# Kernel optimization log

Hardware: AMD Instinct MI355X
Metric: run time of the kernel (lower is better)

## Reference

```python
import jax, jax.numpy as jnp
import numpy as np

B, NUM_OBJ, R, D, C = 1024, 128, 32, 512, 7  # scans, obj slots, rel samples, feat dim, rel classes
N = NUM_OBJ + R  # 160 graph nodes per scan


def setup_inputs() -> dict:
    key = jax.random.key(0)
    ks = jax.random.split(key, 8)
    obj_feats = jax.random.normal(ks[0], (B, NUM_OBJ, D), jnp.float32)
    pairs = jax.random.randint(ks[1], (B, R, 2), 0, NUM_OBJ, dtype=jnp.int32)
    init = lambda k, shape, fan_in: jax.random.normal(k, shape, jnp.float32) / np.float32(np.sqrt(fan_in))
    return {
        "obj_feats": obj_feats,
        "pairs": pairs,
        "fuse_w": init(ks[2], (2 * D, D), 2 * D), "fuse_b": jnp.zeros((D,), jnp.float32),
        "gcn_w": init(ks[3], (D, D), D), "gcn_b": jnp.zeros((D,), jnp.float32),
        "fc1_w": init(ks[4], (D, 256), D), "fc1_b": jnp.zeros((256,), jnp.float32),
        "fc2_w": init(ks[5], (256, 128), 256), "fc2_b": jnp.zeros((128,), jnp.float32),
        "fc3_w": init(ks[6], (128, C), 128), "fc3_b": jnp.zeros((C,), jnp.float32),
    }


def reference(obj_feats, pairs, fuse_w, fuse_b, gcn_w, gcn_b,
              fc1_w, fc1_b, fc2_w, fc2_b, fc3_w, fc3_b):
    # --- init_rel_node (pos_fuse=False): fuse sub/obj features per sampled pair ---
    sub = jnp.take_along_axis(obj_feats, pairs[:, :, 0:1], axis=1)  # [B,R,D]
    obj = jnp.take_along_axis(obj_feats, pairs[:, :, 1:2], axis=1)  # [B,R,D]
    init_rel = jnp.concatenate([sub, obj], axis=-1) @ fuse_w + fuse_b  # [B,R,D]

    # --- X: object node feats in rows [0,NUM_OBJ), rel node feats in rows [NUM_OBJ,N) ---
    X = jnp.concatenate([obj_feats, init_rel], axis=1)  # [B,N,D]

    # --- A: get_graph_gcn_with_rel -- scatter 4 directed edges per pair ---
    b_idx = jnp.arange(B)[:, None]                      # [B,1]
    ridx = NUM_OBJ + jnp.arange(R)[None, :]             # [1,R] rel node index j+num_obj
    p0, p1 = pairs[:, :, 0], pairs[:, :, 1]             # [B,R]
    A = jnp.zeros((B, N, N), jnp.float32)
    A = A.at[b_idx, p0, ridx].set(1.0)
    A = A.at[b_idx, ridx, p1].set(1.0)
    A = A.at[b_idx, p1, ridx].set(1.0)
    A = A.at[b_idx, ridx, p0].set(1.0)

    # --- simpleGCN: relu((A @ X) W + b) ---
    H = jax.nn.relu(jnp.einsum('bnm,bmd->bnd', A, X) @ gcn_w + gcn_b)  # [B,N,D]

    # --- residual: GCN rel-node output + init rel feats ---
    rel_feat = H[:, NUM_OBJ:, :] + init_rel  # [B,R,D]

    # --- proxi_detector (dropout = identity, eval behavior) ---
    h = jax.nn.relu(rel_feat @ fc1_w + fc1_b)
    h = jax.nn.relu(h @ fc2_w + fc2_b)
    logits = h @ fc3_w + fc3_b  # [B,R,C]
    return jax.nn.softmax(logits, axis=-1)
```

## Files before the change

### kernel.cpp

```cpp
#include <hip/hip_runtime.h>
#include <hip/hip_bf16.h>

#define B_    1024
#define NOBJ  128
#define RREL  32
#define DIM   512
#define MTOT  32768

typedef __bf16 bf16x8 __attribute__((ext_vector_type(8)));
typedef float  f32x4  __attribute__((ext_vector_type(4)));
typedef unsigned short us;

__device__ __forceinline__ us f2bf(float f) {
    unsigned int u = __float_as_uint(f);
    u += 0x7FFFu + ((u >> 16) & 1u);
    return (us)(u >> 16);
}
__device__ __forceinline__ float bf2f(us h) {
    return __uint_as_float(((unsigned int)h) << 16);
}

__device__ __forceinline__ void load16_to_lds(const us* g, us* l) {
    __builtin_amdgcn_global_load_lds((const __attribute__((address_space(1))) void*)g,
                                     (__attribute__((address_space(3))) void*)l,
                                     16, 0, 0);
}

__global__ __launch_bounds__(256) void gather_kernel(
        const float* __restrict__ obj, const int* __restrict__ pairs,
        us* __restrict__ As, us* __restrict__ Msum) {
    int t = threadIdx.x;
    int g = t >> 7;
    int c = t & 127;
    int base = blockIdx.x * 8;
#pragma unroll
    for (int rr = 0; rr < 4; ++rr) {
        int m  = base + rr * 2 + g;
        int b  = m >> 5;
        int p0 = pairs[(m << 1) + 0];
        int p1 = pairs[(m << 1) + 1];
        const float4* srow = (const float4*)(obj + (size_t)(b * NOBJ + p0) * DIM);
        const float4* orow = (const float4*)(obj + (size_t)(b * NOBJ + p1) * DIM);
        float4 s4 = srow[c];
        float4 o4 = orow[c];
        size_t arow = (size_t)m * 1024;
        ushort4 sb = make_ushort4(f2bf(s4.x), f2bf(s4.y), f2bf(s4.z), f2bf(s4.w));
        ushort4 ob = make_ushort4(f2bf(o4.x), f2bf(o4.y), f2bf(o4.z), f2bf(o4.w));
        *(ushort4*)(As + arow + c * 4)       = sb;
        *(ushort4*)(As + arow + 512 + c * 4) = ob;
        float4 mz = s4;
        if (p0 != p1) { mz.x += o4.x; mz.y += o4.y; mz.z += o4.z; mz.w += o4.w; }
        *(ushort4*)(Msum + (size_t)m * 512 + c * 4) =
            make_ushort4(f2bf(mz.x), f2bf(mz.y), f2bf(mz.z), f2bf(mz.w));
    }
}

__global__ __launch_bounds__(256) void prep_weights(
        const float* __restrict__ fw, const float* __restrict__ gw,
        const float* __restrict__ w1, const float* __restrict__ w2,
        us* __restrict__ WfT, us* __restrict__ WgT,
        us* __restrict__ W1T, us* __restrict__ W2T) {
    __shared__ float t32[32][33];
    int id = blockIdx.x;
    const float* in; us* out; int K, N, local;
    if (id < 512)      { in = fw; out = WfT; K = 1024; N = 512; local = id; }
    else if (id < 768) { in = gw; out = WgT; K = 512;  N = 512; local = id - 512; }
    else if (id < 896) { in = w1; out = W1T; K = 512;  N = 256; local = id - 768; }
    else               { in = w2; out = W2T; K = 256;  N = 128; local = id - 896; }
    int tilesN = N >> 5;
    int bk = (local / tilesN) * 32;
    int bn = (local % tilesN) * 32;
    int t  = threadIdx.x;
    int tx = t & 31, ty = t >> 5;
#pragma unroll
    for (int i = 0; i < 4; ++i)
        t32[ty + i * 8][tx] = in[(size_t)(bk + ty + i * 8) * N + bn + tx];
    __syncthreads();
#pragma unroll
    for (int i = 0; i < 4; ++i)
        out[(size_t)(bn + ty + i * 8) * K + bk + tx] = f2bf(t32[tx][ty + i * 8]);
}

__global__ __launch_bounds__(512, 2) void gemm_fused12(
        const us* __restrict__ As,
        const us* __restrict__ Msum,
        const us* __restrict__ WfT,
        const us* __restrict__ WgT,
        const float* __restrict__ fuse_b, const float* __restrict__ gcn_b,
        us* __restrict__ rf) {
    __shared__ __align__(16) us ldsA[2][4096];
    __shared__ __align__(16) us ldsB[2][16384];

    int tid  = threadIdx.x;
    int wid  = tid >> 6;
    int lane = tid & 63;
    int wm   = wid >> 2;
    int wn   = wid & 3;
    int m0   = blockIdx.x * 128;

    f32x4 acc[4][8];
#pragma unroll
    for (int i = 0; i < 4; ++i)
#pragma unroll
        for (int j = 0; j < 8; ++j)
#pragma unroll
            for (int k = 0; k < 4; ++k) acc[i][j][k] = 0.0f;

    int r = tid >> 2, c = tid & 3;
    const us* aG = Msum + (size_t)(m0 + r) * 512  + c * 8;
    const us* aF = As   + (size_t)(m0 + r) * 1024 + c * 8;

    int l15  = lane & 15;
    int koff = (lane >> 4) * 8;
    int aoff = (wm * 64  + l15) * 32 + koff;
    int boff = (wn * 128 + l15) * 32 + koff;

    float bg_[8], bf_[8];
#pragma unroll
    for (int j = 0; j < 8; ++j) {
        int col = wn * 128 + j * 16 + l15;
        bg_[j] = gcn_b[col];
        bf_[j] = fuse_b[col];
    }

    auto stageG = [&](int ks, int buf) {
        load16_to_lds(aG + ks * 32, &ldsA[buf][tid * 8]);
#pragma unroll
        for (int q = 0; q < 4; ++q)
            load16_to_lds(WgT + (size_t)(q * 128 + r) * 512 + ks * 32 + c * 8,
                          &ldsB[buf][q * 4096 + tid * 8]);
    };
    auto stageF = [&](int ks, int buf) {
        load16_to_lds(aF + ks * 32, &ldsA[buf][tid * 8]);
#pragma unroll
        for (int q = 0; q < 4; ++q)
            load16_to_lds(WfT + (size_t)(q * 128 + r) * 1024 + ks * 32 + c * 8,
                          &ldsB[buf][q * 4096 + tid * 8]);
    };
    auto compute = [&](int buf) {
        bf16x8 a[4], b[8];
#pragma unroll
        for (int i = 0; i < 4; ++i)
            a[i] = *(const bf16x8*)(&ldsA[buf][aoff + i * 512]);
#pragma unroll
        for (int j = 0; j < 8; ++j)
            b[j] = *(const bf16x8*)(&ldsB[buf][boff + j * 512]);
#pragma unroll
        for (int i = 0; i < 4; ++i)
#pragma unroll
            for (int j = 0; j < 8; ++j)
                acc[i][j] = __builtin_amdgcn_mfma_f32_16x16x32_bf16(a[i], b[j], acc[i][j], 0, 0, 0);
    };

    int cur = 0;
    stageG(0, 0);
    __syncthreads();

    for (int s = 0; s < 16; ++s) {
        if (s < 15) stageG(s + 1, cur ^ 1);
        else        stageF(0, cur ^ 1);
        compute(cur);
        if (s == 15) {
#pragma unroll
            for (int i = 0; i < 4; ++i)
#pragma unroll
                for (int j = 0; j < 8; ++j)
#pragma unroll
                    for (int k = 0; k < 4; ++k)
                        acc[i][j][k] = fmaxf(acc[i][j][k] + bg_[j], 0.0f);
        }
        __syncthreads();
        cur ^= 1;
    }
    for (int s = 0; s < 32; ++s) {
        if (s < 31) stageF(s + 1, cur ^ 1);
        compute(cur);
        __syncthreads();
        cur ^= 1;
    }

    int crow = wm * 64 + (lane >> 4) * 4;
#pragma unroll
    for (int i = 0; i < 4; ++i)
#pragma unroll
        for (int j = 0; j < 8; ++j) {
            int col = wn * 128 + j * 16 + l15;
#pragma unroll
            for (int jj = 0; jj < 4; ++jj) {
                int row = m0 + crow + i * 16 + jj;
                rf[(size_t)row * 512 + col] = f2bf(acc[i][j][jj] + bf_[j]);
            }
        }
}

#define H1S 264
#define H2S 136
__global__ __launch_bounds__(256, 2) void tail_kernel(
        const us* __restrict__ rf,
        const us* __restrict__ W1T,
        const us* __restrict__ W2T,
        const float* __restrict__ b1, const float* __restrict__ b2,
        const float* __restrict__ w3, const float* __restrict__ b3,
        float* __restrict__ out) {
    __shared__ __align__(16) unsigned char pool[57888];
    us*    sA   = (us*)(pool);
    us*    sB   = (us*)(pool + 4096);
    us*    sH2  = (us*)(pool);
    us*    sH1  = (us*)(pool + 20480);
    float* sRed = (float*)(pool + 20480);
    float* sW3  = (float*)(pool + 54272);
    float* sB3  = (float*)(pool + 57856);

    int tid  = threadIdx.x;
    int wid  = tid >> 6;
    int lane = tid & 63;
    int m0   = blockIdx.x * 64;

    for (int i = tid; i < 128 * 7; i += 256) sW3[i] = w3[i];
    if (tid < 7) sB3[tid] = b3[tid];

    int r = tid >> 2, c = tid & 3;
    int koff = (lane >> 4) * 8;
    int l15  = lane & 15;

    f32x4 acc1[4][4];
#pragma unroll
    for (int i = 0; i < 4; ++i)
#pragma unroll
        for (int j = 0; j < 4; ++j)
#pragma unroll
            for (int k = 0; k < 4; ++k) acc1[i][j][k] = 0.0f;

    {
        const us* ag = rf + (size_t)(m0 + r) * 512 + c * 8;
        us* la = sA + wid * 512;
        for (int k0 = 0; k0 < 512; k0 += 32) {
            __syncthreads();
            load16_to_lds(ag + k0, la);
#pragma unroll
            for (int q = 0; q < 4; ++q)
                load16_to_lds(W1T + (size_t)(q * 64 + r) * 512 + k0 + c * 8,
                              sB + q * 2048 + wid * 512);
            __syncthreads();
            bf16x8 a[4], b[4];
#pragma unroll
            for (int i = 0; i < 4; ++i)
                a[i] = *(const bf16x8*)(sA + (l15 + i * 16) * 32 + koff);
#pragma unroll
            for (int j = 0; j < 4; ++j)
                b[j] = *(const bf16x8*)(sB + (wid * 64 + j * 16 + l15) * 32 + koff);
#pragma unroll
            for (int i = 0; i < 4; ++i)
#pragma unroll
                for (int j = 0; j < 4; ++j)
                    acc1[i][j] = __builtin_amdgcn_mfma_f32_16x16x32_bf16(a[i], b[j], acc1[i][j], 0, 0, 0);
        }
    }
#pragma unroll
    for (int i = 0; i < 4; ++i)
#pragma unroll
        for (int j = 0; j < 4; ++j) {
            int col = wid * 64 + j * 16 + l15;
            float bb = b1[col];
#pragma unroll
            for (int jj = 0; jj < 4; ++jj) {
                int row = i * 16 + (lane >> 4) * 4 + jj;
                sH1[row * H1S + col] = f2bf(fmaxf(acc1[i][j][jj] + bb, 0.0f));
            }
        }

    int nw = wid & 1, kw = wid >> 1;
    f32x4 acc2[4][4];
#pragma unroll
    for (int i = 0; i < 4; ++i)
#pragma unroll
        for (int j = 0; j < 4; ++j)
#pragma unroll
            for (int k = 0; k < 4; ++k) acc2[i][j][k] = 0.0f;

    for (int t = 0; t < 4; ++t) {
        __syncthreads();
#pragma unroll
        for (int s = 0; s < 2; ++s)
#pragma unroll
            for (int q = 0; q < 2; ++q)
                load16_to_lds(W2T + (size_t)(q * 64 + r) * 256 + s * 128 + t * 32 + c * 8,
                              sB + s * 4096 + q * 2048 + wid * 512);
        __syncthreads();
        bf16x8 a[4], b[4];
#pragma unroll
        for (int i = 0; i < 4; ++i)
            a[i] = *(const bf16x8*)(sH1 + (l15 + i * 16) * H1S + kw * 128 + t * 32 + koff);
#pragma unroll
        for (int j = 0; j < 4; ++j)
            b[j] = *(const bf16x8*)(sB + kw * 4096 + (nw * 64 + j * 16 + l15) * 32 + koff);
#pragma unroll
        for (int i = 0; i < 4; ++i)
#pragma unroll
            for (int j = 0; j < 4; ++j)
                acc2[i][j] = __builtin_amdgcn_mfma_f32_16x16x32_bf16(a[i], b[j], acc2[i][j], 0, 0, 0);
    }
    __syncthreads();
    if (kw == 1) {
#pragma unroll
        for (int i = 0; i < 4; ++i)
#pragma unroll
            for (int j = 0; j < 4; ++j) {
                int col = nw * 64 + j * 16 + l15;
#pragma unroll
                for (int jj = 0; jj < 4; ++jj) {
                    int row = i * 16 + (lane >> 4) * 4 + jj;
                    sRed[row * 132 + col] = acc2[i][j][jj];
                }
            }
    }
    __syncthreads();
    if (kw == 0) {
#pragma unroll
        for (int i = 0; i < 4; ++i)
#pragma unroll
            for (int j = 0; j < 4; ++j) {
                int col = nw * 64 + j * 16 + l15;
                float bb = b2[col];
#pragma unroll
                for (int jj = 0; jj < 4; ++jj) {
                    int row = i * 16 + (lane >> 4) * 4 + jj;
                    float v = acc2[i][j][jj] + sRed[row * 132 + col] + bb;
                    sH2[row * H2S + col] = f2bf(fmaxf(v, 0.0f));
                }
            }
    }
    __syncthreads();

    int row = tid >> 2;
    int p   = tid & 3;
    float accv[7];
#pragma unroll
    for (int cc = 0; cc < 7; ++cc) accv[cc] = 0.0f;
    const us* hrow = sH2 + row * H2S + p * 32;
    for (int kk = 0; kk < 8; ++kk) {
        ushort4 u = *(const ushort4*)(hrow + kk * 4);
        float f0 = bf2f(u.x), f1 = bf2f(u.y), f2 = bf2f(u.z), f3 = bf2f(u.w);
        int k = p * 32 + kk * 4;
#pragma unroll
        for (int cc = 0; cc < 7; ++cc) {
            accv[cc] = fmaf(f0, sW3[(k + 0) * 7 + cc], accv[cc]);
            accv[cc] = fmaf(f1, sW3[(k + 1) * 7 + cc], accv[cc]);
            accv[cc] = fmaf(f2, sW3[(k + 2) * 7 + cc], accv[cc]);
            accv[cc] = fmaf(f3, sW3[(k + 3) * 7 + cc], accv[cc]);
        }
    }
#pragma unroll
    for (int cc = 0; cc < 7; ++cc) {
        accv[cc] += __shfl_xor(accv[cc], 1);
        accv[cc] += __shfl_xor(accv[cc], 2);
    }
    if (p == 0) {
        float mx = accv[0] + sB3[0];
        float lg[7];
#pragma unroll
        for (int cc = 0; cc < 7; ++cc) { lg[cc] = accv[cc] + sB3[cc]; mx = fmaxf(mx, lg[cc]); }
        float sum = 0.f;
#pragma unroll
        for (int cc = 0; cc < 7; ++cc) { lg[cc] = __expf(lg[cc] - mx); sum += lg[cc]; }
        float inv = 1.0f / sum;
#pragma unroll
        for (int cc = 0; cc < 7; ++cc) out[(size_t)(m0 + row) * 7 + cc] = lg[cc] * inv;
    }
}

extern "C" void kernel_launch(void* const* d_in, const int* in_sizes, int n_in,
                              void* d_out, int out_size, void* d_ws, size_t ws_size,
                              hipStream_t stream) {
    (void)in_sizes; (void)n_in; (void)out_size; (void)ws_size;
    const float* obj    = (const float*)d_in[0];
    const int*   pairs  = (const int*)  d_in[1];
    const float* fuse_w = (const float*)d_in[2];
    const float* fuse_b = (const float*)d_in[3];
    const float* gcn_w  = (const float*)d_in[4];
    const float* gcn_b  = (const float*)d_in[5];
    const float* fc1_w  = (const float*)d_in[6];
    const float* fc1_b  = (const float*)d_in[7];
    const float* fc2_w  = (const float*)d_in[8];
    const float* fc2_b  = (const float*)d_in[9];
    const float* fc3_w  = (const float*)d_in[10];
    const float* fc3_b  = (const float*)d_in[11];
    float* out = (float*)d_out;

    char* ws = (char*)d_ws;
    us* As   = (us*)(ws);
    us* Msum = (us*)(ws + (64u  << 20));
    us* rf   = (us*)(ws + (96u  << 20));
    us* WfT  = (us*)(ws + (128u << 20));
    us* WgT  = (us*)(ws + (129u << 20));
    us* W1T  = (us*)(ws + (130u << 20));
    us* W2T  = (us*)(ws + (131u << 20));

    gather_kernel<<<MTOT / 8, 256, 0, stream>>>(obj, pairs, As, Msum);
    prep_weights<<<928, 256, 0, stream>>>(fuse_w, gcn_w, fc1_w, fc2_w,
                                          WfT, WgT, W1T, W2T);

    gemm_fused12<<<MTOT / 128, 512, 0, stream>>>(
        As, Msum, WfT, WgT, fuse_b, gcn_b, rf);

    tail_kernel<<<MTOT / 64, 256, 0, stream>>>(
        rf, W1T, W2T, fc1_b, fc2_b, fc3_w, fc3_b, out);
}
```

Before: 444.5 us.

## Fuse pair gather and bf16 conversion into the fused GEMM A-tile loader

Removes the separate gather kernel that wrote bf16 copies of sub/obj rows and their sum to workspace. The GEMM now reads fp32 object rows through the pair indices, converts them to bf16 in registers, and writes them into LDS, with register prefetch one stage ahead. This saves a kernel launch and the round trip of the gathered matrices through global memory. In exchange the A loads become fp32 register loads plus conversion work inside the GEMM loop instead of async global-to-LDS copies, which may expose latency.

Result: faster. 425.8 us (-4.2%).

```diff
diff --git a/kernel.cpp b/kernel.cpp
--- a/kernel.cpp
+++ b/kernel.cpp
@@ -10,6 +10,7 @@
 typedef __bf16 bf16x8 __attribute__((ext_vector_type(8)));
 typedef float  f32x4  __attribute__((ext_vector_type(4)));
 typedef unsigned short us;
+typedef unsigned short us8v __attribute__((ext_vector_type(8)));
 
 __device__ __forceinline__ us f2bf(float f) {
     unsigned int u = __float_as_uint(f);
@@ -24,35 +25,6 @@
     __builtin_amdgcn_global_load_lds((const __attribute__((address_space(1))) void*)g,
                                      (__attribute__((address_space(3))) void*)l,
                                      16, 0, 0);
-}
-
-__global__ __launch_bounds__(256) void gather_kernel(
-        const float* __restrict__ obj, const int* __restrict__ pairs,
-        us* __restrict__ As, us* __restrict__ Msum) {
-    int t = threadIdx.x;
-    int g = t >> 7;
-    int c = t & 127;
-    int base = blockIdx.x * 8;
-#pragma unroll
-    for (int rr = 0; rr < 4; ++rr) {
-        int m  = base + rr * 2 + g;
-        int b  = m >> 5;
-        int p0 = pairs[(m << 1) + 0];
-        int p1 = pairs[(m << 1) + 1];
-        const float4* srow = (const float4*)(obj + (size_t)(b * NOBJ + p0) * DIM);
-        const float4* orow = (const float4*)(obj + (size_t)(b * NOBJ + p1) * DIM);
-        float4 s4 = srow[c];
-        float4 o4 = orow[c];
-        size_t arow = (size_t)m * 1024;
-        ushort4 sb = make_ushort4(f2bf(s4.x), f2bf(s4.y), f2bf(s4.z), f2bf(s4.w));
-        ushort4 ob = make_ushort4(f2bf(o4.x), f2bf(o4.y), f2bf(o4.z), f2bf(o4.w));
-        *(ushort4*)(As + arow + c * 4)       = sb;
-        *(ushort4*)(As + arow + 512 + c * 4) = ob;
-        float4 mz = s4;
-        if (p0 != p1) { mz.x += o4.x; mz.y += o4.y; mz.z += o4.z; mz.w += o4.w; }
-        *(ushort4*)(Msum + (size_t)m * 512 + c * 4) =
-            make_ushort4(f2bf(mz.x), f2bf(mz.y), f2bf(mz.z), f2bf(mz.w));
-    }
 }
 
 __global__ __launch_bounds__(256) void prep_weights(
@@ -82,8 +54,8 @@
 }
 
 __global__ __launch_bounds__(512, 2) void gemm_fused12(
-        const us* __restrict__ As,
-        const us* __restrict__ Msum,
+        const float* __restrict__ obj,
+        const int*   __restrict__ pairs,
         const us* __restrict__ WfT,
         const us* __restrict__ WgT,
         const float* __restrict__ fuse_b, const float* __restrict__ gcn_b,
@@ -107,8 +79,13 @@
             for (int k = 0; k < 4; ++k) acc[i][j][k] = 0.0f;
 
     int r = tid >> 2, c = tid & 3;
-    const us* aG = Msum + (size_t)(m0 + r) * 512  + c * 8;
-    const us* aF = As   + (size_t)(m0 + r) * 1024 + c * 8;
+    int m  = m0 + r;
+    int p0 = pairs[2 * m + 0];
+    int p1 = pairs[2 * m + 1];
+    int bi = m >> 5;
+    const float* sP = obj + (size_t)(bi * NOBJ + p0) * DIM + c * 8;
+    const float* oP = obj + (size_t)(bi * NOBJ + p1) * DIM + c * 8;
+    float osc = (p0 != p1) ? 1.0f : 0.0f;
 
     int l15  = lane & 15;
     int koff = (lane >> 4) * 8;
@@ -123,20 +100,9 @@
         bf_[j] = fuse_b[col];
     }
 
-    auto stageG = [&](int ks, int buf) {
-        load16_to_lds(aG + ks * 32, &ldsA[buf][tid * 8]);
-#pragma unroll
-        for (int q = 0; q < 4; ++q)
-            load16_to_lds(WgT + (size_t)(q * 128 + r) * 512 + ks * 32 + c * 8,
-                          &ldsB[buf][q * 4096 + tid * 8]);
-    };
-    auto stageF = [&](int ks, int buf) {
-        load16_to_lds(aF + ks * 32, &ldsA[buf][tid * 8]);
-#pragma unroll
-        for (int q = 0; q < 4; ++q)
-            load16_to_lds(WfT + (size_t)(q * 128 + r) * 1024 + ks * 32 + c * 8,
-                          &ldsB[buf][q * 4096 + tid * 8]);
-    };
+    us* aDst0 = &ldsA[0][r * 32 + c * 8];
+    us* aDst1 = &ldsA[1][r * 32 + c * 8];
+
     auto compute = [&](int buf) {
         bf16x8 a[4], b[8];
 #pragma unroll
@@ -152,15 +118,56 @@
                 acc[i][j] = __builtin_amdgcn_mfma_f32_16x16x32_bf16(a[i], b[j], acc[i][j], 0, 0, 0);
     };
 
+    {
+        float4 sa = *(const float4*)(sP);
+        float4 sb = *(const float4*)(sP + 4);
+        float4 oa = *(const float4*)(oP);
+        float4 ob = *(const float4*)(oP + 4);
+        us8v u;
+        u[0] = f2bf(fmaf(osc, oa.x, sa.x)); u[1] = f2bf(fmaf(osc, oa.y, sa.y));
+        u[2] = f2bf(fmaf(osc, oa.z, sa.z)); u[3] = f2bf(fmaf(osc, oa.w, sa.w));
+        u[4] = f2bf(fmaf(osc, ob.x, sb.x)); u[5] = f2bf(fmaf(osc, ob.y, sb.y));
+        u[6] = f2bf(fmaf(osc, ob.z, sb.z)); u[7] = f2bf(fmaf(osc, ob.w, sb.w));
+        *(us8v*)aDst0 = u;
+#pragma unroll
+        for (int q = 0; q < 4; ++q)
+            load16_to_lds(WgT + (size_t)(q * 128 + r) * 512 + c * 8,
+                          &ldsB[0][q * 4096 + tid * 8]);
+    }
+    __syncthreads();
+
     int cur = 0;
-    stageG(0, 0);
-    __syncthreads();
-
-    for (int s = 0; s < 16; ++s) {
-        if (s < 15) stageG(s + 1, cur ^ 1);
-        else        stageF(0, cur ^ 1);
+    for (int t = 0; t < 48; ++t) {
+        float4 ra, rb, rc, rd;
+        int  nt = t + 1;
+        bool hv = nt < 48;
+        bool gm = nt < 16;
+        if (hv) {
+            if (gm) {
+                int k0 = nt * 32;
+                ra = *(const float4*)(sP + k0);
+                rb = *(const float4*)(sP + k0 + 4);
+                rc = *(const float4*)(oP + k0);
+                rd = *(const float4*)(oP + k0 + 4);
+#pragma unroll
+                for (int q = 0; q < 4; ++q)
+                    load16_to_lds(WgT + (size_t)(q * 128 + r) * 512 + k0 + c * 8,
+                                  &ldsB[cur ^ 1][q * 4096 + tid * 8]);
+            } else {
+                int kf = (nt - 16) * 32;
+                const float* p = (kf < 512) ? (sP + kf) : (oP + (kf - 512));
+                ra = *(const float4*)(p);
+                rb = *(const float4*)(p + 4);
+#pragma unroll
+                for (int q = 0; q < 4; ++q)
+                    load16_to_lds(WfT + (size_t)(q * 128 + r) * 1024 + kf + c * 8,
+                                  &ldsB[cur ^ 1][q * 4096 + tid * 8]);
+            }
+        }
+
         compute(cur);
-        if (s == 15) {
+
+        if (t == 15) {
 #pragma unroll
             for (int i = 0; i < 4; ++i)
 #pragma unroll
@@ -169,12 +176,20 @@
                     for (int k = 0; k < 4; ++k)
                         acc[i][j][k] = fmaxf(acc[i][j][k] + bg_[j], 0.0f);
         }
-        __syncthreads();
-        cur ^= 1;
-    }
-    for (int s = 0; s < 32; ++s) {
-        if (s < 31) stageF(s + 1, cur ^ 1);
-        compute(cur);
+
+        if (hv) {
+            us8v u;
+            if (gm) {
+                u[0] = f2bf(fmaf(osc, rc.x, ra.x)); u[1] = f2bf(fmaf(osc, rc.y, ra.y));
+                u[2] = f2bf(fmaf(osc, rc.z, ra.z)); u[3] = f2bf(fmaf(osc, rc.w, ra.w));
+                u[4] = f2bf(fmaf(osc, rd.x, rb.x)); u[5] = f2bf(fmaf(osc, rd.y, rb.y));
+                u[6] = f2bf(fmaf(osc, rd.z, rb.z)); u[7] = f2bf(fmaf(osc, rd.w, rb.w));
+            } else {
+                u[0] = f2bf(ra.x); u[1] = f2bf(ra.y); u[2] = f2bf(ra.z); u[3] = f2bf(ra.w);
+                u[4] = f2bf(rb.x); u[5] = f2bf(rb.y); u[6] = f2bf(rb.z); u[7] = f2bf(rb.w);
+            }
+            *(us8v*)((cur == 0) ? aDst1 : aDst0) = u;
+        }
         __syncthreads();
         cur ^= 1;
     }
@@ -388,20 +403,17 @@
     float* out = (float*)d_out;
 
     char* ws = (char*)d_ws;
-    us* As   = (us*)(ws);
-    us* Msum = (us*)(ws + (64u  << 20));
-    us* rf   = (us*)(ws + (96u  << 20));
-    us* WfT  = (us*)(ws + (128u << 20));
-    us* WgT  = (us*)(ws + (129u << 20));
-    us* W1T  = (us*)(ws + (130u << 20));
-    us* W2T  = (us*)(ws + (131u << 20));
-
-    gather_kernel<<<MTOT / 8, 256, 0, stream>>>(obj, pairs, As, Msum);
+    us* rf   = (us*)(ws);
+    us* WfT  = (us*)(ws + (32u << 20));
+    us* WgT  = (us*)(ws + (33u << 20));
+    us* W1T  = (us*)(ws + (34u << 20));
+    us* W2T  = (us*)(ws + (35u << 20));
+
     prep_weights<<<928, 256, 0, stream>>>(fuse_w, gcn_w, fc1_w, fc2_w,
                                           WfT, WgT, W1T, W2T);
 
     gemm_fused12<<<MTOT / 128, 512, 0, stream>>>(
-        As, Msum, WfT, WgT, fuse_b, gcn_b, rf);
+        obj, pairs, WfT, WgT, fuse_b, gcn_b, rf);
 
     tail_kernel<<<MTOT / 64, 256, 0, stream>>>(
         rf, W1T, W2T, fc1_b, fc2_b, fc3_w, fc3_b, out);
```
